# Kernel tuning notes

Measured on AMD Instinct MI355X. Metric: run time of the kernel, lower is better.

## Reference

```python
import jax, jax.numpy as jnp
import numpy as np
import math

B, R, Q, K, C = 1, 128, 256, 256, 256
H, D = 8, 32  # no_heads, c_hidden; H*D == C


def setup_inputs() -> dict:
    key = jax.random.key(0)
    ks = jax.random.split(key, 11)
    s = 0.02
    return {
        "q_x": jax.random.normal(ks[0], (B, R, Q, C), jnp.float32),
        "k_x": jax.random.normal(ks[1], (B, R, K, C), jnp.float32),
        "v_x": jax.random.normal(ks[2], (B, R, K, C), jnp.float32),
        "bias": jax.random.normal(ks[3], (1, 1, H, Q, K), jnp.float32),
        # weights stored [in, out] (equivalent to torch Linear weight.T)
        "Wq": jax.random.normal(ks[4], (C, H * D), jnp.float32) * s,
        "Wk": jax.random.normal(ks[5], (C, H * D), jnp.float32) * s,
        "Wv": jax.random.normal(ks[6], (C, H * D), jnp.float32) * s,
        "Wo": jax.random.normal(ks[7], (H * D, C), jnp.float32) * s,
        "bo": jax.random.normal(ks[8], (C,), jnp.float32) * s,
        "Wg": jax.random.normal(ks[9], (C, H * D), jnp.float32) * s,
        "bg": jnp.ones((H * D,), jnp.float32),  # gating init: bias = 1
    }


def reference(q_x, k_x, v_x, bias, Wq, Wk, Wv, Wo, bo, Wg, bg):
    norm = 1.0 / math.sqrt(D)
    # projections -> [*, S, H, D]
    q = (q_x @ Wq).reshape(*q_x.shape[:-1], H, D)
    k = (k_x @ Wk).reshape(*k_x.shape[:-1], H, D)
    v = (v_x @ Wv).reshape(*v_x.shape[:-1], H, D)
    # scaled logits [*, H, Q, K] plus external bias
    a = jnp.einsum("...qhd,...khd->...hqk", q, k) * norm + bias
    a = jax.nn.softmax(a, axis=-1)
    # [*, Q, H, D]
    o = jnp.einsum("...hqk,...khd->...qhd", a, v)
    # sigmoid gate from query data
    g = jax.nn.sigmoid(q_x @ Wg + bg).reshape(o.shape)
    o = o * g
    o = o.reshape(*o.shape[:-2], H * D)
    return o @ Wo + bo
```

## Files before the change

### kernel.cpp

```cpp
#include <hip/hip_runtime.h>
#include <hip/hip_bf16.h>
#include <cstdint>
#include <cstddef>

typedef __attribute__((ext_vector_type(8))) short short8;
typedef __attribute__((ext_vector_type(4))) short s16x4;
typedef __attribute__((ext_vector_type(4))) unsigned short u16x4;
typedef __attribute__((ext_vector_type(4))) float f32x4;
typedef __attribute__((ext_vector_type(4))) unsigned int u32x4;

__device__ __forceinline__ short bfbits(float f) {
    __bf16 h = (__bf16)f;
    return __builtin_bit_cast(short, h);
}
__device__ __forceinline__ float bf2f(unsigned short b) {
    union { uint32_t u; float f; } v; v.u = ((uint32_t)b) << 16;
    return v.f;
}
__device__ __forceinline__ unsigned int pack2(float x, float y) {
    return (unsigned int)(unsigned short)bfbits(x) |
           ((unsigned int)(unsigned short)bfbits(y) << 16);
}

__global__ __launch_bounds__(256) void wt_kernel(
    const float* __restrict__ Wq, const float* __restrict__ Wk,
    const float* __restrict__ Wv, const float* __restrict__ Wg,
    const float* __restrict__ Wo, unsigned short* __restrict__ wt)
{
    int mat  = blockIdx.x >> 4;
    int tile = blockIdx.x & 15;
    int k0 = (tile >> 2) * 64, n0 = (tile & 3) * 64;
    const float* W = (mat==0)?Wq:(mat==1)?Wk:(mat==2)?Wv:(mat==3)?Wg:Wo;
    __shared__ unsigned short T[64][72];
    int tid = threadIdx.x;
    int tx = tid & 15, ty = tid >> 4;
    #pragma unroll
    for (int j = 0; j < 4; ++j) {
        int kr = ty + j*16;
        f32x4 v = *(const f32x4*)(W + (size_t)(k0+kr)*256 + n0 + tx*4);
        #pragma unroll
        for (int e = 0; e < 4; ++e) T[tx*4+e][kr] = (unsigned short)bfbits(v[e]);
    }
    __syncthreads();
    #pragma unroll
    for (int j = 0; j < 4; ++j) {
        int nr = ty + j*16;
        u16x4 st;
        #pragma unroll
        for (int e = 0; e < 4; ++e) st[e] = T[nr][tx*4+e];
        *(u16x4*)(wt + ((size_t)mat*256 + n0+nr)*256 + k0 + tx*4) = st;
    }
}

__global__ __launch_bounds__(256) void bias_prep_kernel(
    const float* __restrict__ bias, float* __restrict__ bt)
{
    int hb = blockIdx.x;
    int h = hb >> 4, qt = hb & 15;
    int tid = threadIdx.x;
    int cc = tid >> 4, n = tid & 15;
    const float* src = bias + ((size_t)(h*256 + qt*16 + cc))*256 + n*16;
    float* dst = bt + ((size_t)(hb*16 + n))*256 + cc*16;
    #pragma unroll
    for (int q = 0; q < 4; ++q)
        *(f32x4*)(dst + q*4) = *(const f32x4*)(src + q*4);
}

template<int SWAP>
__device__ __forceinline__ void proj_mfma_loop(
    const unsigned short* As, const unsigned short* Wt,
    int col0, int c, int g, f32x4 acc[4][4])
{
    short8 pb[4];
    #pragma unroll
    for (int n = 0; n < 4; ++n)
        pb[n] = *(const short8*)(Wt + (size_t)(col0 + n*16 + c) * 256 + g*8);

    #pragma unroll
    for (int step = 0; step < 8; ++step) {
        short8 b[4];
        #pragma unroll
        for (int n = 0; n < 4; ++n) b[n] = pb[n];
        if (step < 7) {
            int koff = (step + 1) * 32 + g * 8;
            #pragma unroll
            for (int n = 0; n < 4; ++n)
                pb[n] = *(const short8*)(Wt + (size_t)(col0 + n*16 + c) * 256 + koff);
        }
        short8 a[4];
        #pragma unroll
        for (int m = 0; m < 4; ++m) {
            int row = m * 16 + c;
            int off = row * 512 + ((step * 64 + g * 16) ^ ((row & 31) << 4));
            a[m] = *(const short8*)((const char*)As + off);
        }
        #pragma unroll
        for (int m = 0; m < 4; ++m)
            #pragma unroll
            for (int n = 0; n < 4; ++n) {
                if (SWAP)
                    acc[m][n] = __builtin_amdgcn_mfma_f32_16x16x32_bf16(b[n], a[m], acc[m][n], 0, 0, 0);
                else
                    acc[m][n] = __builtin_amdgcn_mfma_f32_16x16x32_bf16(a[m], b[n], acc[m][n], 0, 0, 0);
            }
    }
}

__global__ __launch_bounds__(256) void proj_kernel(
    const float* __restrict__ qx, const float* __restrict__ kx, const float* __restrict__ vx,
    const float* __restrict__ bg, const unsigned short* __restrict__ wt,
    unsigned short* __restrict__ Qa, unsigned short* __restrict__ Ka,
    unsigned short* __restrict__ Va, unsigned short* __restrict__ G)
{
    __shared__ __align__(16) unsigned short As[64 * 256];

    int bx = blockIdx.x;
    int p  = bx & 3;
    int rb = bx >> 2;
    int row0 = rb * 64;
    int tid = threadIdx.x;
    int lane = tid & 63;
    int c = lane & 15, g = lane >> 4;
    int col0 = (tid >> 6) * 64;

    const float* X = (p == 1) ? kx : (p == 2) ? vx : qx;
    const unsigned short* Wt = wt + (size_t)p * 65536;

    {
        int l32 = tid & 31;
        int rg  = tid >> 5;
        #pragma unroll
        for (int j = 0; j < 8; ++j) {
            int row = j * 8 + rg;
            const float* src = X + (size_t)(row0 + row) * 256 + l32 * 8;
            f32x4 lo = *(const f32x4*)src;
            f32x4 hi = *(const f32x4*)(src + 4);
            u32x4 pkv;
            pkv[0] = pack2(lo[0], lo[1]); pkv[1] = pack2(lo[2], lo[3]);
            pkv[2] = pack2(hi[0], hi[1]); pkv[3] = pack2(hi[2], hi[3]);
            int off = row * 512 + ((l32 * 16) ^ ((row & 31) << 4));
            *(u32x4*)((char*)As + off) = pkv;
        }
    }
    __syncthreads();

    f32x4 acc[4][4];
    #pragma unroll
    for (int m = 0; m < 4; ++m)
        #pragma unroll
        for (int n = 0; n < 4; ++n)
            acc[m][n] = 0.0f;

    if (p == 2) proj_mfma_loop<0>(As, Wt, col0, c, g, acc);
    else        proj_mfma_loop<1>(As, Wt, col0, c, g, acc);

    int r_ = row0 >> 8;
    int s0base = row0 & 255;

    if (p == 2) {
        #pragma unroll
        for (int m = 0; m < 4; ++m) {
            int s0 = s0base + m * 16 + 4 * g;
            #pragma unroll
            for (int n = 0; n < 4; ++n) {
                int dcol = col0 + n * 16 + c;
                int h_ = dcol >> 5, d_ = dcol & 31;
                u16x4 st;
                #pragma unroll
                for (int i = 0; i < 4; ++i) st[i] = (unsigned short)bfbits(acc[m][n][i]);
                *(u16x4*)(Va + ((size_t)((r_*8 + h_)*32 + d_)) * 256 + s0) = st;
            }
        }
    } else if (p == 3) {
        #pragma unroll
        for (int n = 0; n < 4; ++n) {
            int colb = col0 + n * 16 + 4 * g;
            f32x4 bgv = *(const f32x4*)(bg + colb);
            #pragma unroll
            for (int m = 0; m < 4; ++m) {
                int rq = row0 + m * 16 + c;
                u16x4 st;
                #pragma unroll
                for (int i = 0; i < 4; ++i) {
                    float s = 1.0f / (1.0f + __expf(-(acc[m][n][i] + bgv[i])));
                    st[i] = (unsigned short)bfbits(s);
                }
                *(u16x4*)(G + (size_t)rq * 256 + colb) = st;
            }
        }
    } else {
        unsigned short* dst = p ? Ka : Qa;
        #pragma unroll
        for (int n = 0; n < 4; ++n) {
            int colb = col0 + n * 16 + 4 * g;
            int h_ = colb >> 5, d0 = colb & 31;
            #pragma unroll
            for (int m = 0; m < 4; ++m) {
                int s_ = s0base + m * 16 + c;
                u16x4 st;
                #pragma unroll
                for (int i = 0; i < 4; ++i) st[i] = (unsigned short)bfbits(acc[m][n][i]);
                *(u16x4*)(dst + ((size_t)((r_*8 + h_)*256 + s_)) * 32 + d0) = st;
            }
        }
    }
}

__global__ __launch_bounds__(512) void attn_kernel(
    const unsigned short* __restrict__ Qa, const unsigned short* __restrict__ Ka,
    const unsigned short* __restrict__ Va, const unsigned short* __restrict__ G,
    const float* __restrict__ bt, unsigned short* __restrict__ og)
{
    __shared__ __align__(16) unsigned short Ks[256 * 40];
    __shared__ __align__(16) unsigned short Vs[32 * 264];

    int rh = blockIdx.x;
    int r = rh >> 3, h = rh & 7;
    int tid = threadIdx.x;
    int w = tid >> 6, lane = tid & 63;
    int c = lane & 15, g = lane >> 4;
    size_t base = (size_t)rh * 8192;

    #pragma unroll
    for (int j = 0; j < 2; ++j) {
        int idx8 = (tid + j*512) * 8;
        int s_ = idx8 >> 5, d_ = idx8 & 31;
        short8 v = *(const short8*)(Ka + base + idx8);
        *(short8*)(&Ks[s_*40 + d_]) = v;
    }
    #pragma unroll
    for (int j = 0; j < 2; ++j) {
        int idx8 = (tid + j*512) * 8;
        int d_ = idx8 >> 8, s0 = idx8 & 255;
        short8 v = *(const short8*)(Va + base + idx8);
        int t  = s0 >> 5;
        int ap = (s0 >> 3) & 3;
        int bb = ap >> 1;
        int g1 = (2*ap) & 3, g2 = (2*ap + 1) & 3;
        int p1 = t*32 + g1*8 + 4*bb;
        int p2 = t*32 + g2*8 + 4*bb;
        s16x4 lo, hi;
        lo[0]=v[0]; lo[1]=v[1]; lo[2]=v[2]; lo[3]=v[3];
        hi[0]=v[4]; hi[1]=v[5]; hi[2]=v[6]; hi[3]=v[7];
        *(s16x4*)(&Vs[d_*264 + p1]) = lo;
        *(s16x4*)(&Vs[d_*264 + p2]) = hi;
    }
    __syncthreads();

    const float* bth = bt + (size_t)h * 65536;
    const float nrmv = 0.17677669529663687f;

    #pragma unroll 1
    for (int qq = 0; qq < 2; ++qq) {
        int qt = w*2 + qq;
        int qrow = qt * 16;
        short8 qf = *(const short8*)(Qa + base + (size_t)(qrow + c)*32 + g*8);
        const float* btt = bth + (size_t)qt*4096 + (c*4 + g)*4;

        f32x4 o0 = 0.0f, o1 = 0.0f;
        float sum = 0.f;
        #pragma unroll
        for (int t = 0; t < 8; ++t) {
            int n0 = 2*t, n1 = 2*t + 1;
            short8 kf0 = *(const short8*)(&Ks[(n0*16 + c)*40 + g*8]);
            short8 kf1 = *(const short8*)(&Ks[(n1*16 + c)*40 + g*8]);
            f32x4 bv0 = *(const f32x4*)(btt + n0*256);
            f32x4 bv1 = *(const f32x4*)(btt + n1*256);
            f32x4 z = 0.0f;
            f32x4 s0 = __builtin_amdgcn_mfma_f32_16x16x32_bf16(kf0, qf, z, 0, 0, 0);
            f32x4 s1 = __builtin_amdgcn_mfma_f32_16x16x32_bf16(kf1, qf, z, 0, 0, 0);
            float e0 = __expf(fmaf(s0[0], nrmv, bv0[0]));
            float e1 = __expf(fmaf(s0[1], nrmv, bv0[1]));
            float e2 = __expf(fmaf(s0[2], nrmv, bv0[2]));
            float e3 = __expf(fmaf(s0[3], nrmv, bv0[3]));
            float e4 = __expf(fmaf(s1[0], nrmv, bv1[0]));
            float e5 = __expf(fmaf(s1[1], nrmv, bv1[1]));
            float e6 = __expf(fmaf(s1[2], nrmv, bv1[2]));
            float e7 = __expf(fmaf(s1[3], nrmv, bv1[3]));
            sum += ((e0+e1)+(e2+e3)) + ((e4+e5)+(e6+e7));
            u32x4 aw;
            aw[0] = pack2(e0, e1); aw[1] = pack2(e2, e3);
            aw[2] = pack2(e4, e5); aw[3] = pack2(e6, e7);
            short8 pfrag = __builtin_bit_cast(short8, aw);
            short8 va0 = *(const short8*)(&Vs[(c)*264      + t*32 + g*8]);
            short8 va1 = *(const short8*)(&Vs[(16 + c)*264 + t*32 + g*8]);
            o0 = __builtin_amdgcn_mfma_f32_16x16x32_bf16(va0, pfrag, o0, 0, 0, 0);
            o1 = __builtin_amdgcn_mfma_f32_16x16x32_bf16(va1, pfrag, o1, 0, 0, 0);
        }
        sum += __shfl_xor(sum, 16);
        sum += __shfl_xor(sum, 32);
        float inv = 1.0f / sum;

        size_t orow = ((size_t)(r*256 + qrow + c)) * 256 + h*32;
        #pragma unroll
        for (int n2 = 0; n2 < 2; ++n2) {
            int d0 = n2*16 + 4*g;
            u16x4 gv = *(const u16x4*)(G + orow + d0);
            f32x4 ov = n2 ? o1 : o0;
            u16x4 st;
            #pragma unroll
            for (int i = 0; i < 4; ++i)
                st[i] = (unsigned short)bfbits(ov[i] * inv * bf2f(gv[i]));
            *(u16x4*)(og + orow + d0) = st;
        }
    }
}

__global__ __launch_bounds__(256) void oproj_kernel(
    const unsigned short* __restrict__ og, const unsigned short* __restrict__ wt_o,
    const float* __restrict__ bo, float* __restrict__ out)
{
    __shared__ __align__(16) unsigned short As[64 * 256];

    int row0 = blockIdx.x * 64;
    int tid = threadIdx.x;
    int lane = tid & 63;
    int c = lane & 15, g = lane >> 4;
    int col0 = (tid >> 6) * 64;

    #pragma unroll
    for (int j = 0; j < 8; ++j) {
        int idx = tid * 8 + j * 2048;
        int row = idx >> 8;
        int colB = (idx & 255) * 2;
        short8 v = *(const short8*)(og + (size_t)(row0 + row) * 256 + (idx & 255));
        int off = row * 512 + (colB ^ ((row & 31) << 4));
        *(short8*)((char*)As + off) = v;
    }
    __syncthreads();

    f32x4 acc[4][4];
    #pragma unroll
    for (int m = 0; m < 4; ++m)
        #pragma unroll
        for (int n = 0; n < 4; ++n)
            acc[m][n] = 0.0f;

    proj_mfma_loop<1>(As, wt_o, col0, c, g, acc);

    #pragma unroll
    for (int n = 0; n < 4; ++n) {
        int colb = col0 + n * 16 + 4 * g;
        f32x4 bov = *(const f32x4*)(bo + colb);
        #pragma unroll
        for (int m = 0; m < 4; ++m) {
            int row = row0 + m * 16 + c;
            f32x4 st = acc[m][n] + bov;
            *(f32x4*)(out + (size_t)row * 256 + colb) = st;
        }
    }
}

extern "C" void kernel_launch(void* const* d_in, const int* in_sizes, int n_in,
                              void* d_out, int out_size, void* d_ws, size_t ws_size,
                              hipStream_t stream) {
    const float* qx   = (const float*)d_in[0];
    const float* kx   = (const float*)d_in[1];
    const float* vx   = (const float*)d_in[2];
    const float* bias = (const float*)d_in[3];
    const float* Wq   = (const float*)d_in[4];
    const float* Wk   = (const float*)d_in[5];
    const float* Wv   = (const float*)d_in[6];
    const float* Wo   = (const float*)d_in[7];
    const float* bo   = (const float*)d_in[8];
    const float* Wg   = (const float*)d_in[9];
    const float* bg   = (const float*)d_in[10];

    uint8_t* ws = (uint8_t*)d_ws;
    unsigned short* wt = (unsigned short*)ws;
    unsigned short* Qa = (unsigned short*)(ws + (1u<<20));
    unsigned short* Ka = (unsigned short*)(ws + (1u<<20) + 1u*(1u<<24));
    unsigned short* Va = (unsigned short*)(ws + (1u<<20) + 2u*(1u<<24));
    unsigned short* G  = (unsigned short*)(ws + (1u<<20) + 3u*(1u<<24));
    unsigned short* og = (unsigned short*)(ws + (1u<<20) + 4u*(1u<<24));
    float*          bt = (float*)        (ws + (1u<<20) + 5u*(1u<<24));

    hipLaunchKernelGGL(wt_kernel, dim3(80), dim3(256), 0, stream, Wq, Wk, Wv, Wg, Wo, wt);
    hipLaunchKernelGGL(bias_prep_kernel, dim3(128), dim3(256), 0, stream, bias, bt);
    hipLaunchKernelGGL(proj_kernel, dim3(2048), dim3(256), 0, stream, qx, kx, vx, bg, wt, Qa, Ka, Va, G);
    hipLaunchKernelGGL(attn_kernel, dim3(1024), dim3(512), 0, stream, Qa, Ka, Va, G, bt, og);
    hipLaunchKernelGGL(oproj_kernel, dim3(512), dim3(256), 0, stream, og, wt + 4*65536, bo, (float*)d_out);
}
```

Measured before the change: 133.3 us.

## Pipeline projection input loads through double-buffered K-chunks of shared memory

The projection kernel now stages the fp32 input tile in 64-column chunks into two small shared buffers instead of converting the whole 64x256 tile up front. Global loads for the next chunk are issued before the MFMAs on the current chunk, so the load latency can overlap with compute. Shared memory per block drops from 32KB to 16KB, which may allow more resident blocks. The cost is extra barriers per chunk and more live registers for the prefetched data.

```diff
diff --git a/kernel.cpp b/kernel.cpp
--- a/kernel.cpp
+++ b/kernel.cpp
@@ -66,8 +66,7 @@
         *(f32x4*)(dst + q*4) = *(const f32x4*)(src + q*4);
 }
 
-template<int SWAP>
-__device__ __forceinline__ void proj_mfma_loop(
+__device__ __forceinline__ void proj_mfma_loop_swap(
     const unsigned short* As, const unsigned short* Wt,
     int col0, int c, int g, f32x4 acc[4][4])
 {
@@ -97,12 +96,8 @@
         #pragma unroll
         for (int m = 0; m < 4; ++m)
             #pragma unroll
-            for (int n = 0; n < 4; ++n) {
-                if (SWAP)
-                    acc[m][n] = __builtin_amdgcn_mfma_f32_16x16x32_bf16(b[n], a[m], acc[m][n], 0, 0, 0);
-                else
-                    acc[m][n] = __builtin_amdgcn_mfma_f32_16x16x32_bf16(a[m], b[n], acc[m][n], 0, 0, 0);
-            }
+            for (int n = 0; n < 4; ++n)
+                acc[m][n] = __builtin_amdgcn_mfma_f32_16x16x32_bf16(b[n], a[m], acc[m][n], 0, 0, 0);
     }
 }
 
@@ -112,7 +107,7 @@
     unsigned short* __restrict__ Qa, unsigned short* __restrict__ Ka,
     unsigned short* __restrict__ Va, unsigned short* __restrict__ G)
 {
-    __shared__ __align__(16) unsigned short As[64 * 256];
+    __shared__ __align__(16) unsigned short Asb[2][64 * 64];
 
     int bx = blockIdx.x;
     int p  = bx & 3;
@@ -126,21 +121,29 @@
     const float* X = (p == 1) ? kx : (p == 2) ? vx : qx;
     const unsigned short* Wt = wt + (size_t)p * 65536;
 
+    int srow = tid >> 2;
+    int sk0  = (tid & 3) * 16;
+    const float* xrow = X + (size_t)(row0 + srow) * 256 + sk0;
+    int wb0 = srow * 128 + ((sk0 * 2)      ^ ((srow & 7) << 4));
+    int wb1 = srow * 128 + ((sk0 * 2 + 16) ^ ((srow & 7) << 4));
+
+    short8 pb[4];
+    #pragma unroll
+    for (int n = 0; n < 4; ++n)
+        pb[n] = *(const short8*)(Wt + (size_t)(col0 + n*16 + c) * 256 + g*8);
+
     {
-        int l32 = tid & 31;
-        int rg  = tid >> 5;
-        #pragma unroll
-        for (int j = 0; j < 8; ++j) {
-            int row = j * 8 + rg;
-            const float* src = X + (size_t)(row0 + row) * 256 + l32 * 8;
-            f32x4 lo = *(const f32x4*)src;
-            f32x4 hi = *(const f32x4*)(src + 4);
-            u32x4 pkv;
-            pkv[0] = pack2(lo[0], lo[1]); pkv[1] = pack2(lo[2], lo[3]);
-            pkv[2] = pack2(hi[0], hi[1]); pkv[3] = pack2(hi[2], hi[3]);
-            int off = row * 512 + ((l32 * 16) ^ ((row & 31) << 4));
-            *(u32x4*)((char*)As + off) = pkv;
-        }
+        f32x4 x0 = *(const f32x4*)(xrow + 0);
+        f32x4 x1 = *(const f32x4*)(xrow + 4);
+        f32x4 x2 = *(const f32x4*)(xrow + 8);
+        f32x4 x3 = *(const f32x4*)(xrow + 12);
+        u32x4 w0, w1;
+        w0[0]=pack2(x0[0],x0[1]); w0[1]=pack2(x0[2],x0[3]);
+        w0[2]=pack2(x1[0],x1[1]); w0[3]=pack2(x1[2],x1[3]);
+        w1[0]=pack2(x2[0],x2[1]); w1[1]=pack2(x2[2],x2[3]);
+        w1[2]=pack2(x3[0],x3[1]); w1[3]=pack2(x3[2],x3[3]);
+        *(u32x4*)((char*)&Asb[0][0] + wb0) = w0;
+        *(u32x4*)((char*)&Asb[0][0] + wb1) = w1;
     }
     __syncthreads();
 
@@ -151,8 +154,60 @@
         for (int n = 0; n < 4; ++n)
             acc[m][n] = 0.0f;
 
-    if (p == 2) proj_mfma_loop<0>(As, Wt, col0, c, g, acc);
-    else        proj_mfma_loop<1>(As, Wt, col0, c, g, acc);
+    #pragma unroll
+    for (int ch = 0; ch < 4; ++ch) {
+        f32x4 x0, x1, x2, x3;
+        if (ch < 3) {
+            const float* src = xrow + (ch + 1) * 64;
+            x0 = *(const f32x4*)(src + 0);
+            x1 = *(const f32x4*)(src + 4);
+            x2 = *(const f32x4*)(src + 8);
+            x3 = *(const f32x4*)(src + 12);
+        }
+
+        const unsigned short* As = &Asb[ch & 1][0];
+        #pragma unroll
+        for (int s = 0; s < 2; ++s) {
+            int step = ch * 2 + s;
+            short8 b[4];
+            #pragma unroll
+            for (int n = 0; n < 4; ++n) b[n] = pb[n];
+            if (step < 7) {
+                int koff = (step + 1) * 32 + g * 8;
+                #pragma unroll
+                for (int n = 0; n < 4; ++n)
+                    pb[n] = *(const short8*)(Wt + (size_t)(col0 + n*16 + c) * 256 + koff);
+            }
+            short8 a[4];
+            #pragma unroll
+            for (int m = 0; m < 4; ++m) {
+                int row = m * 16 + c;
+                int off = row * 128 + ((s * 64 + g * 16) ^ ((row & 7) << 4));
+                a[m] = *(const short8*)((const char*)As + off);
+            }
+            #pragma unroll
+            for (int m = 0; m < 4; ++m)
+                #pragma unroll
+                for (int n = 0; n < 4; ++n) {
+                    if (p == 2)
+                        acc[m][n] = __builtin_amdgcn_mfma_f32_16x16x32_bf16(a[m], b[n], acc[m][n], 0, 0, 0);
+                    else
+                        acc[m][n] = __builtin_amdgcn_mfma_f32_16x16x32_bf16(b[n], a[m], acc[m][n], 0, 0, 0);
+                }
+        }
+        __syncthreads();
+        if (ch < 3) {
+            u32x4 w0, w1;
+            w0[0]=pack2(x0[0],x0[1]); w0[1]=pack2(x0[2],x0[3]);
+            w0[2]=pack2(x1[0],x1[1]); w0[3]=pack2(x1[2],x1[3]);
+            w1[0]=pack2(x2[0],x2[1]); w1[1]=pack2(x2[2],x2[3]);
+            w1[2]=pack2(x3[0],x3[1]); w1[3]=pack2(x3[2],x3[3]);
+            char* dst = (char*)&Asb[(ch + 1) & 1][0];
+            *(u32x4*)(dst + wb0) = w0;
+            *(u32x4*)(dst + wb1) = w1;
+            __syncthreads();
+        }
+    }
 
     int r_ = row0 >> 8;
     int s0base = row0 & 255;
@@ -336,7 +391,7 @@
         for (int n = 0; n < 4; ++n)
             acc[m][n] = 0.0f;
 
-    proj_mfma_loop<1>(As, wt_o, col0, c, g, acc);
+    proj_mfma_loop_swap(As, wt_o, col0, c, g, acc);
 
     #pragma unroll
     for (int n = 0; n < 4; ++n) {
```

Result: no change. 134.4 us (+0.8%).

## Merge prep kernels, reuse q_x tile for gate projection, widen stores

Applied to the files above, without the earlier changes.

Merges the weight-transpose and bias-prep kernels into one launch. In the projection kernel, each q_x block now runs both the Q and gate projections from the same staged tile, so q_x is loaded and converted once and the grid shrinks from four to three block types. Q/K/V/G outputs are written as 8-wide bf16 stores by permuting the output column order, with matching changes to the V shared-memory staging, the gate read in attention, and the Wo row permutation that compensates for the new og layout. The cost is longer-running Q blocks, which can cause load imbalance.

```diff
diff --git a/kernel.cpp b/kernel.cpp
--- a/kernel.cpp
+++ b/kernel.cpp
@@ -6,6 +6,7 @@
 typedef __attribute__((ext_vector_type(8))) short short8;
 typedef __attribute__((ext_vector_type(4))) short s16x4;
 typedef __attribute__((ext_vector_type(4))) unsigned short u16x4;
+typedef __attribute__((ext_vector_type(8))) unsigned short u16x8;
 typedef __attribute__((ext_vector_type(4))) float f32x4;
 typedef __attribute__((ext_vector_type(4))) unsigned int u32x4;
 
@@ -22,48 +23,54 @@
            ((unsigned int)(unsigned short)bfbits(y) << 16);
 }
 
-__global__ __launch_bounds__(256) void wt_kernel(
+__global__ __launch_bounds__(256) void prep_kernel(
     const float* __restrict__ Wq, const float* __restrict__ Wk,
     const float* __restrict__ Wv, const float* __restrict__ Wg,
-    const float* __restrict__ Wo, unsigned short* __restrict__ wt)
-{
-    int mat  = blockIdx.x >> 4;
-    int tile = blockIdx.x & 15;
-    int k0 = (tile >> 2) * 64, n0 = (tile & 3) * 64;
-    const float* W = (mat==0)?Wq:(mat==1)?Wk:(mat==2)?Wv:(mat==3)?Wg:Wo;
-    __shared__ unsigned short T[64][72];
+    const float* __restrict__ Wo, unsigned short* __restrict__ wt,
+    const float* __restrict__ bias, float* __restrict__ bt)
+{
+    int bid = blockIdx.x;
     int tid = threadIdx.x;
-    int tx = tid & 15, ty = tid >> 4;
-    #pragma unroll
-    for (int j = 0; j < 4; ++j) {
-        int kr = ty + j*16;
-        f32x4 v = *(const f32x4*)(W + (size_t)(k0+kr)*256 + n0 + tx*4);
-        #pragma unroll
-        for (int e = 0; e < 4; ++e) T[tx*4+e][kr] = (unsigned short)bfbits(v[e]);
-    }
-    __syncthreads();
-    #pragma unroll
-    for (int j = 0; j < 4; ++j) {
-        int nr = ty + j*16;
-        u16x4 st;
-        #pragma unroll
-        for (int e = 0; e < 4; ++e) st[e] = T[nr][tx*4+e];
-        *(u16x4*)(wt + ((size_t)mat*256 + n0+nr)*256 + k0 + tx*4) = st;
-    }
-}
-
-__global__ __launch_bounds__(256) void bias_prep_kernel(
-    const float* __restrict__ bias, float* __restrict__ bt)
-{
-    int hb = blockIdx.x;
-    int h = hb >> 4, qt = hb & 15;
-    int tid = threadIdx.x;
-    int cc = tid >> 4, n = tid & 15;
-    const float* src = bias + ((size_t)(h*256 + qt*16 + cc))*256 + n*16;
-    float* dst = bt + ((size_t)(hb*16 + n))*256 + cc*16;
-    #pragma unroll
-    for (int q = 0; q < 4; ++q)
-        *(f32x4*)(dst + q*4) = *(const f32x4*)(src + q*4);
+    if (bid < 80) {
+        int mat  = bid >> 4;
+        int tile = bid & 15;
+        int k0 = (tile >> 2) * 64, n0 = (tile & 3) * 64;
+        const float* W = (mat==0)?Wq:(mat==1)?Wk:(mat==2)?Wv:(mat==3)?Wg:Wo;
+        __shared__ unsigned short T[64][72];
+        int tx = tid & 15, ty = tid >> 4;
+        #pragma unroll
+        for (int j = 0; j < 4; ++j) {
+            int kr = ty + j*16;
+            f32x4 v = *(const f32x4*)(W + (size_t)(k0+kr)*256 + n0 + tx*4);
+            #pragma unroll
+            for (int e = 0; e < 4; ++e) T[tx*4+e][kr] = (unsigned short)bfbits(v[e]);
+        }
+        __syncthreads();
+        #pragma unroll
+        for (int j = 0; j < 4; ++j) {
+            int nr = ty + j*16;
+            int kk = k0 + tx*4;
+            int dstk = kk;
+            if (mat == 4) {
+                int a = (kk >> 2) & 7;
+                int hb = kk & ~31;
+                dstk = hb + ((a < 4) ? 8*a : 8*(a-4) + 4);
+            }
+            u16x4 st;
+            #pragma unroll
+            for (int e = 0; e < 4; ++e) st[e] = T[nr][tx*4+e];
+            *(u16x4*)(wt + ((size_t)mat*256 + n0+nr)*256 + dstk) = st;
+        }
+    } else {
+        int hb = bid - 80;
+        int h = hb >> 4, qt = hb & 15;
+        int cc = tid >> 4, n = tid & 15;
+        const float* src = bias + ((size_t)(h*256 + qt*16 + cc))*256 + n*16;
+        float* dst = bt + ((size_t)(hb*16 + n))*256 + cc*16;
+        #pragma unroll
+        for (int q = 0; q < 4; ++q)
+            *(f32x4*)(dst + q*4) = *(const f32x4*)(src + q*4);
+    }
 }
 
 template<int SWAP>
@@ -115,16 +122,15 @@
     __shared__ __align__(16) unsigned short As[64 * 256];
 
     int bx = blockIdx.x;
-    int p  = bx & 3;
-    int rb = bx >> 2;
+    int typ = bx % 3;
+    int rb  = bx / 3;
     int row0 = rb * 64;
     int tid = threadIdx.x;
     int lane = tid & 63;
     int c = lane & 15, g = lane >> 4;
     int col0 = (tid >> 6) * 64;
 
-    const float* X = (p == 1) ? kx : (p == 2) ? vx : qx;
-    const unsigned short* Wt = wt + (size_t)p * 65536;
+    const float* X = (typ == 0) ? qx : (typ == 1) ? kx : vx;
 
     {
         int l32 = tid & 31;
@@ -144,63 +150,79 @@
     }
     __syncthreads();
 
+    int r_ = row0 >> 8;
+    int s0b = row0 & 255;
+
     f32x4 acc[4][4];
     #pragma unroll
     for (int m = 0; m < 4; ++m)
         #pragma unroll
-        for (int n = 0; n < 4; ++n)
-            acc[m][n] = 0.0f;
-
-    if (p == 2) proj_mfma_loop<0>(As, Wt, col0, c, g, acc);
-    else        proj_mfma_loop<1>(As, Wt, col0, c, g, acc);
-
-    int r_ = row0 >> 8;
-    int s0base = row0 & 255;
-
-    if (p == 2) {
-        #pragma unroll
-        for (int m = 0; m < 4; ++m) {
-            int s0 = s0base + m * 16 + 4 * g;
-            #pragma unroll
-            for (int n = 0; n < 4; ++n) {
-                int dcol = col0 + n * 16 + c;
-                int h_ = dcol >> 5, d_ = dcol & 31;
-                u16x4 st;
-                #pragma unroll
-                for (int i = 0; i < 4; ++i) st[i] = (unsigned short)bfbits(acc[m][n][i]);
-                *(u16x4*)(Va + ((size_t)((r_*8 + h_)*32 + d_)) * 256 + s0) = st;
-            }
-        }
-    } else if (p == 3) {
+        for (int n = 0; n < 4; ++n) acc[m][n] = 0.0f;
+
+    if (typ == 2) {
+        proj_mfma_loop<0>(As, wt + 2*65536, col0, c, g, acc);
         #pragma unroll
         for (int n = 0; n < 4; ++n) {
-            int colb = col0 + n * 16 + 4 * g;
-            f32x4 bgv = *(const f32x4*)(bg + colb);
-            #pragma unroll
-            for (int m = 0; m < 4; ++m) {
-                int rq = row0 + m * 16 + c;
-                u16x4 st;
+            int dcol = col0 + n * 16;
+            int h_ = dcol >> 5, d_ = (dcol & 31) + c;
+            size_t rowbase = ((size_t)((r_*8 + h_)*32 + d_)) * 256;
+            #pragma unroll
+            for (int p = 0; p < 2; ++p) {
+                u16x8 st;
                 #pragma unroll
                 for (int i = 0; i < 4; ++i) {
-                    float s = 1.0f / (1.0f + __expf(-(acc[m][n][i] + bgv[i])));
-                    st[i] = (unsigned short)bfbits(s);
+                    st[i]     = (unsigned short)bfbits(acc[2*p][n][i]);
+                    st[i + 4] = (unsigned short)bfbits(acc[2*p+1][n][i]);
                 }
-                *(u16x4*)(G + (size_t)rq * 256 + colb) = st;
+                *(u16x8*)(Va + rowbase + s0b + 32*p + 8*g) = st;
             }
         }
     } else {
-        unsigned short* dst = p ? Ka : Qa;
-        #pragma unroll
-        for (int n = 0; n < 4; ++n) {
-            int colb = col0 + n * 16 + 4 * g;
-            int h_ = colb >> 5, d0 = colb & 31;
+        const unsigned short* WtA = (typ == 0) ? wt : wt + 65536;
+        proj_mfma_loop<1>(As, WtA, col0, c, g, acc);
+        unsigned short* dst = (typ == 0) ? Qa : Ka;
+        #pragma unroll
+        for (int np = 0; np < 2; ++np) {
+            int n0 = 2 * np;
+            int h_ = (col0 + n0*16) >> 5;
             #pragma unroll
             for (int m = 0; m < 4; ++m) {
-                int s_ = s0base + m * 16 + c;
-                u16x4 st;
+                int s_ = s0b + m * 16 + c;
+                u16x8 st;
                 #pragma unroll
-                for (int i = 0; i < 4; ++i) st[i] = (unsigned short)bfbits(acc[m][n][i]);
-                *(u16x4*)(dst + ((size_t)((r_*8 + h_)*256 + s_)) * 32 + d0) = st;
+                for (int i = 0; i < 4; ++i) {
+                    st[i]     = (unsigned short)bfbits(acc[m][n0][i]);
+                    st[i + 4] = (unsigned short)bfbits(acc[m][n0+1][i]);
+                }
+                *(u16x8*)(dst + ((size_t)((r_*8 + h_)*256 + s_)) * 32 + 8*g) = st;
+            }
+        }
+
+        if (typ == 0) {
+            #pragma unroll
+            for (int m = 0; m < 4; ++m)
+                #pragma unroll
+                for (int n = 0; n < 4; ++n) acc[m][n] = 0.0f;
+            proj_mfma_loop<1>(As, wt + 3*65536, col0, c, g, acc);
+            #pragma unroll
+            for (int np = 0; np < 2; ++np) {
+                int n0 = 2 * np;
+                int colb = col0 + n0 * 16;
+                f32x4 bg0 = *(const f32x4*)(bg + colb + 4*g);
+                f32x4 bg1 = *(const f32x4*)(bg + colb + 16 + 4*g);
+                #pragma unroll
+                for (int m = 0; m < 4; ++m) {
+                    int rq = row0 + m * 16 + c;
+                    u16x8 st;
+                    #pragma unroll
+                    for (int i = 0; i < 4; ++i) {
+                        float sa = 1.0f / (1.0f + __expf(-(acc[m][n0][i]   + bg0[i])));
+                        float sb = 1.0f / (1.0f + __expf(-(acc[m][n0+1][i] + bg1[i])));
+                        st[i]     = (unsigned short)bfbits(sa);
+                        st[i + 4] = (unsigned short)bfbits(sb);
+                    }
+                    *(u16x8*)(G + (size_t)rq * 256 + colb + 8*g) = st;
+                }
             }
         }
     }
@@ -233,17 +255,7 @@
         int idx8 = (tid + j*512) * 8;
         int d_ = idx8 >> 8, s0 = idx8 & 255;
         short8 v = *(const short8*)(Va + base + idx8);
-        int t  = s0 >> 5;
-        int ap = (s0 >> 3) & 3;
-        int bb = ap >> 1;
-        int g1 = (2*ap) & 3, g2 = (2*ap + 1) & 3;
-        int p1 = t*32 + g1*8 + 4*bb;
-        int p2 = t*32 + g2*8 + 4*bb;
-        s16x4 lo, hi;
-        lo[0]=v[0]; lo[1]=v[1]; lo[2]=v[2]; lo[3]=v[3];
-        hi[0]=v[4]; hi[1]=v[5]; hi[2]=v[6]; hi[3]=v[7];
-        *(s16x4*)(&Vs[d_*264 + p1]) = lo;
-        *(s16x4*)(&Vs[d_*264 + p2]) = hi;
+        *(short8*)(&Vs[d_*264 + s0]) = v;
     }
     __syncthreads();
 
@@ -291,18 +303,50 @@
         sum += __shfl_xor(sum, 32);
         float inv = 1.0f / sum;
 
-        size_t orow = ((size_t)(r*256 + qrow + c)) * 256 + h*32;
-        #pragma unroll
-        for (int n2 = 0; n2 < 2; ++n2) {
-            int d0 = n2*16 + 4*g;
-            u16x4 gv = *(const u16x4*)(G + orow + d0);
-            f32x4 ov = n2 ? o1 : o0;
-            u16x4 st;
-            #pragma unroll
-            for (int i = 0; i < 4; ++i)
-                st[i] = (unsigned short)bfbits(ov[i] * inv * bf2f(gv[i]));
-            *(u16x4*)(og + orow + d0) = st;
-        }
+        size_t orow = ((size_t)(r*256 + qrow + c)) * 256 + h*32 + 8*g;
+        u16x8 gv = *(const u16x8*)(G + orow);
+        u16x8 st;
+        #pragma unroll
+        for (int i = 0; i < 4; ++i) {
+            st[i]     = (unsigned short)bfbits(o0[i] * inv * bf2f(gv[i]));
+            st[i + 4] = (unsigned short)bfbits(o1[i] * inv * bf2f(gv[i + 4]));
+        }
+        *(u16x8*)(og + orow) = st;
+    }
+}
+
+__device__ __forceinline__ void proj_mfma_loop_swap(
+    const unsigned short* As, const unsigned short* Wt,
+    int col0, int c, int g, f32x4 acc[4][4])
+{
+    short8 pb[4];
+    #pragma unroll
+    for (int n = 0; n < 4; ++n)
+        pb[n] = *(const short8*)(Wt + (size_t)(col0 + n*16 + c) * 256 + g*8);
+
+    #pragma unroll
+    for (int step = 0; step < 8; ++step) {
+        short8 b[4];
+        #pragma unroll
+        for (int n = 0; n < 4; ++n) b[n] = pb[n];
+        if (step < 7) {
+            int koff = (step + 1) * 32 + g * 8;
+            #pragma unroll
+            for (int n = 0; n < 4; ++n)
+                pb[n] = *(const short8*)(Wt + (size_t)(col0 + n*16 + c) * 256 + koff);
+        }
+        short8 a[4];
+        #pragma unroll
+        for (int m = 0; m < 4; ++m) {
+            int row = m * 16 + c;
+            int off = row * 512 + ((step * 64 + g * 16) ^ ((row & 31) << 4));
+            a[m] = *(const short8*)((const char*)As + off);
+        }
+        #pragma unroll
+        for (int m = 0; m < 4; ++m)
+            #pragma unroll
+            for (int n = 0; n < 4; ++n)
+                acc[m][n] = __builtin_amdgcn_mfma_f32_16x16x32_bf16(b[n], a[m], acc[m][n], 0, 0, 0);
     }
 }
 
@@ -336,7 +380,7 @@
         for (int n = 0; n < 4; ++n)
             acc[m][n] = 0.0f;
 
-    proj_mfma_loop<1>(As, wt_o, col0, c, g, acc);
+    proj_mfma_loop_swap(As, wt_o, col0, c, g, acc);
 
     #pragma unroll
     for (int n = 0; n < 4; ++n) {
@@ -375,9 +419,12 @@
     unsigned short* og = (unsigned short*)(ws + (1u<<20) + 4u*(1u<<24));
     float*          bt = (float*)        (ws + (1u<<20) + 5u*(1u<<24));
 
-    hipLaunchKernelGGL(wt_kernel, dim3(80), dim3(256), 0, stream, Wq, Wk, Wv, Wg, Wo, wt);
-    hipLaunchKernelGGL(bias_prep_kernel, dim3(128), dim3(256), 0, stream, bias, bt);
-    hipLaunchKernelGGL(proj_kernel, dim3(2048), dim3(256), 0, stream, qx, kx, vx, bg, wt, Qa, Ka, Va, G);
-    hipLaunchKernelGGL(attn_kernel, dim3(1024), dim3(512), 0, stream, Qa, Ka, Va, G, bt, og);
-    hipLaunchKernelGGL(oproj_kernel, dim3(512), dim3(256), 0, stream, og, wt + 4*65536, bo, (float*)d_out);
-}
+    hipLaunchKernelGGL(prep_kernel, dim3(208), dim3(256), 0, stream,
+                       Wq, Wk, Wv, Wg, Wo, wt, bias, bt);
+    hipLaunchKernelGGL(proj_kernel, dim3(1536), dim3(256), 0, stream,
+                       qx, kx, vx, bg, wt, Qa, Ka, Va, G);
+    hipLaunchKernelGGL(attn_kernel, dim3(1024), dim3(512), 0, stream,
+                       Qa, Ka, Va, G, bt, og);
+    hipLaunchKernelGGL(oproj_kernel, dim3(512), dim3(256), 0, stream,
+                       og, wt + 4*65536, bo, (float*)d_out);
+}
```

Measured after the change: 120.9 us. -9.3%, faster.
